# Optimization experiments

Hardware: AMD Instinct MI355X
Metric: run time of the kernel (lower is better)

Reference implementation:

```python
import jax, jax.numpy as jnp
import numpy as np
from jax import lax

DN = ('NCHW', 'OIHW', 'NCHW')

def conv3x3(x, w):
    return lax.conv_general_dilated(x, w, (1, 1), 'SAME', dimension_numbers=DN)

def conv1x1(x, w, b):
    # w: [O, C], x: [B, C, H, W]
    return jnp.einsum('oc,bchw->bohw', w, x) + b[None, :, None, None]

def bn_relu(x, p):
    # p: [2, C] -> (scale, shift), eval-mode folded BatchNorm + ReLU
    return jax.nn.relu(x * p[0][None, :, None, None] + p[1][None, :, None, None])

def pam(y, Wb, bb, Wc, bc, Wd, bd, alpha):
    B, C, H, W = y.shape
    n = H * W
    b_ = conv1x1(y, Wb, bb).reshape(B, -1, n)   # [B, C/8, N]
    c_ = conv1x1(y, Wc, bc).reshape(B, -1, n)   # [B, C/8, N]
    d_ = conv1x1(y, Wd, bd).reshape(B, C, n)    # [B, C, N]
    energy = jnp.einsum('bkn,bkm->bnm', b_, c_)  # [B, N, N]
    attn = jax.nn.softmax(energy, axis=-1)
    feat = jnp.einsum('bcm,bnm->bcn', d_, attn).reshape(B, C, H, W)
    return alpha[0] * feat + y

def cam(y, beta):
    B, C, H, W = y.shape
    xf = y.reshape(B, C, H * W)
    energy = jnp.einsum('bcn,bdn->bcd', xf, xf)  # [B, C, C]
    energy = jnp.max(energy, axis=-1, keepdims=True) - energy
    attn = jax.nn.softmax(energy, axis=-1)
    feat = jnp.einsum('bcd,bdn->bcn', attn, xf).reshape(B, C, H, W)
    return beta[0] * feat + y

def reference(x, Wp1, bnp1, Wc1, bnc1, Wb, bb, Wc, bc, Wd, bd, alpha, beta,
              Wp2, bnp2, Wc2, bnc2, Wout, bout, Wp3, bp3, Wc3, bc3):
    feat_p = bn_relu(conv3x3(x, Wp1), bnp1)
    feat_p = pam(feat_p, Wb, bb, Wc, bc, Wd, bd, alpha)
    feat_p = bn_relu(conv3x3(feat_p, Wp2), bnp2)

    feat_c = bn_relu(conv3x3(x, Wc1), bnc1)
    feat_c = cam(feat_c, beta)
    feat_c = bn_relu(conv3x3(feat_c, Wc2), bnc2)

    fusion = feat_p + feat_c
    out_main = jax.nn.sigmoid(conv1x1(fusion, Wout, bout))
    out_p = jax.nn.sigmoid(conv1x1(feat_p, Wp3, bp3))
    out_c = jax.nn.sigmoid(conv1x1(feat_c, Wc3, bc3))
    return (out_main, out_p, out_c)

def setup_inputs() -> dict:
    key = jax.random.key(0)
    ks = jax.random.split(key, 24)
    Cin, Ci, Ck, NC = 512, 128, 16, 19
    B, H, W = 8, 64, 64
    s = lambda k, shape, scale=0.05: jax.random.normal(k, shape, jnp.float32) * scale
    return {
        'x': jax.random.normal(ks[0], (B, Cin, H, W), jnp.float32),
        'Wp1': s(ks[1], (Ci, Cin, 3, 3)), 'bnp1': jnp.stack([jnp.ones(Ci), jnp.zeros(Ci)]),
        'Wc1': s(ks[2], (Ci, Cin, 3, 3)), 'bnc1': jnp.stack([jnp.ones(Ci), jnp.zeros(Ci)]),
        'Wb': s(ks[3], (Ck, Ci)), 'bb': s(ks[4], (Ck,)),
        'Wc': s(ks[5], (Ck, Ci)), 'bc': s(ks[6], (Ck,)),
        'Wd': s(ks[7], (Ci, Ci)), 'bd': s(ks[8], (Ci,)),
        'alpha': jax.random.normal(ks[9], (1,), jnp.float32) * 0.5,
        'beta': jax.random.normal(ks[10], (1,), jnp.float32) * 0.5,
        'Wp2': s(ks[11], (Ci, Ci, 3, 3)), 'bnp2': jnp.stack([jnp.ones(Ci), jnp.zeros(Ci)]),
        'Wc2': s(ks[12], (Ci, Ci, 3, 3)), 'bnc2': jnp.stack([jnp.ones(Ci), jnp.zeros(Ci)]),
        'Wout': s(ks[13], (NC, Ci)), 'bout': s(ks[14], (NC,)),
        'Wp3': s(ks[15], (NC, Ci)), 'bp3': s(ks[16], (NC,)),
        'Wc3': s(ks[17], (NC, Ci)), 'bc3': s(ks[18], (NC,)),
    }
```

## Files before the change

### kernel.cpp

```cpp
#include <hip/hip_runtime.h>
#include <math.h>


typedef __attribute__((ext_vector_type(8)))  short short8;
typedef __attribute__((ext_vector_type(16))) float f32x16;

__device__ inline unsigned short f2bf(float f) {
    union { float f; unsigned u; } v; v.f = f;
    unsigned r = v.u + 0x7fffu + ((v.u >> 16) & 1u);
    return (unsigned short)(r >> 16);
}
__device__ inline float bf2f(unsigned short h) {
    union { unsigned u; float f; } v; v.u = ((unsigned)h) << 16;
    return v.f;
}

__global__ __launch_bounds__(256) void wpack_kernel(
    const float* __restrict__ W, unsigned short* __restrict__ wp, int Cin, int total)
{
    int idx = blockIdx.x * 256 + threadIdx.x;
    if (idx >= total) return;
    int chunk = idx / 18432;
    int rem   = idx - chunk * 18432;
    int tap   = rem >> 11;
    int rem2  = rem & 2047;
    int g     = rem2 >> 10;
    int co    = (rem2 >> 3) & 127;
    int ci8   = rem2 & 7;
    int cin   = (chunk << 4) + (g << 3) + ci8;
    wp[idx] = f2bf(W[((size_t)co * Cin + cin) * 9 + tap]);
}

__global__ __launch_bounds__(256) void wpack_split_kernel(
    const float* __restrict__ W, unsigned short* __restrict__ wph,
    unsigned short* __restrict__ wpl, int Cin, int total)
{
    int idx = blockIdx.x * 256 + threadIdx.x;
    if (idx >= total) return;
    int chunk = idx / 18432;
    int rem   = idx - chunk * 18432;
    int tap   = rem >> 11;
    int rem2  = rem & 2047;
    int g     = rem2 >> 10;
    int co    = (rem2 >> 3) & 127;
    int ci8   = rem2 & 7;
    int cin   = (chunk << 4) + (g << 3) + ci8;
    float w = W[((size_t)co * Cin + cin) * 9 + tap];
    unsigned short hi = f2bf(w);
    wph[idx] = hi;
    wpl[idx] = f2bf(w - bf2f(hi));
}

__global__ __launch_bounds__(256, 4) void conv3x3_merged(
    const float* __restrict__ xin,
    const unsigned short* __restrict__ wpp,
    const unsigned short* __restrict__ wph, const unsigned short* __restrict__ wpl,
    const float* __restrict__ bnp, const float* __restrict__ bnc,
    float* __restrict__ outP, float* __restrict__ outC,
    unsigned short* __restrict__ outh, unsigned short* __restrict__ outl)
{
    const int t   = threadIdx.x;
    const int w2  = t >> 6;
    const int xh  = w2 & 1;
    const int wy  = w2 >> 1;
    const int ln  = t & 63;
    const int l31 = ln & 31;
    const int g   = ln >> 5;
    const int y   = blockIdx.x;
    const int co0 = blockIdx.y << 6;
    const int b   = blockIdx.z;

    const int sr   = t >> 6;
    const int sx   = t & 63;
    const int sgy  = y - 1 + sr;
    const bool sv  = (t < 192) && ((unsigned)sgy < 64u);
    const int spid = sr * 66 + sx + 1;

    __shared__ __align__(16) unsigned short Xh[2][3168];
    __shared__ __align__(16) unsigned short Xo[2][3168];

    for (int i = t; i < 792; i += 256) {
        uint4 z; z.x = 0; z.y = 0; z.z = 0; z.w = 0;
        ((uint4*)Xh)[i] = z;
        ((uint4*)Xo)[i] = z;
    }

    const int co = co0 + (wy << 5) + l31;
    const unsigned short* wPb = wpp + (size_t)(g << 10) + ((size_t)co << 3);
    const unsigned short* wHb = wph + (size_t)(g << 10) + ((size_t)co << 3);
    const unsigned short* wLb = wpl + (size_t)(g << 10) + ((size_t)co << 3);
    const float* xsrc = xin + ((size_t)b << 21) + (sgy << 6) + sx;

    const f32x16 zero = {0,0,0,0,0,0,0,0,0,0,0,0,0,0,0,0};
    f32x16 ap = zero, ac = zero;

    float xv[16];
    if (sv) {
#pragma unroll
        for (int c = 0; c < 16; c++) xv[c] = xsrc[(size_t)c << 12];
    }
    __syncthreads();

    if (sv) {
        unsigned short th[16], tl[16];
#pragma unroll
        for (int c = 0; c < 16; c++) {
            unsigned short hi = f2bf(xv[c]);
            th[c] = hi; tl[c] = f2bf(xv[c] - bf2f(hi));
        }
        *(uint4*)&Xh[0][spid << 3]          = ((uint4*)th)[0];
        *(uint4*)&Xh[0][1584 + (spid << 3)] = ((uint4*)th)[1];
        *(uint4*)&Xo[0][spid << 3]          = ((uint4*)tl)[0];
        *(uint4*)&Xo[0][1584 + (spid << 3)] = ((uint4*)tl)[1];
    }

    int cur = 0;
    for (int ch = 0; ch < 32; ++ch) {
        __syncthreads();
        const bool pf = (ch < 31);
        if (pf && sv) {
#pragma unroll
            for (int c = 0; c < 16; c++)
                xv[c] = xsrc[((size_t)(ch + 1) << 16) + ((size_t)c << 12)];
        }
        const size_t wo = (size_t)ch * 18432;
#pragma unroll 3
        for (int tap = 0; tap < 9; ++tap) {
            const int dy = tap / 3, dx = tap - dy * 3;
            const int xi = (g ? 1584 : 0) + (((dy * 66) + (xh << 5) + l31 + dx) << 3);
            short8 vap = *(const short8*)(wPb + wo + tap * 2048);
            short8 vah = *(const short8*)(wHb + wo + tap * 2048);
            short8 val = *(const short8*)(wLb + wo + tap * 2048);
            short8 bh_ = *(const short8*)&Xh[cur][xi];
            short8 bl_ = *(const short8*)&Xo[cur][xi];
            ap = __builtin_amdgcn_mfma_f32_32x32x16_bf16(vap, bh_, ap, 0, 0, 0);
            ac = __builtin_amdgcn_mfma_f32_32x32x16_bf16(vah, bh_, ac, 0, 0, 0);
            ac = __builtin_amdgcn_mfma_f32_32x32x16_bf16(vah, bl_, ac, 0, 0, 0);
            ac = __builtin_amdgcn_mfma_f32_32x32x16_bf16(val, bh_, ac, 0, 0, 0);
        }
        if (pf && sv) {
            unsigned short th[16], tl[16];
#pragma unroll
            for (int c = 0; c < 16; c++) {
                unsigned short hi = f2bf(xv[c]);
                th[c] = hi; tl[c] = f2bf(xv[c] - bf2f(hi));
            }
            const int nb = cur ^ 1;
            *(uint4*)&Xh[nb][spid << 3]          = ((uint4*)th)[0];
            *(uint4*)&Xh[nb][1584 + (spid << 3)] = ((uint4*)th)[1];
            *(uint4*)&Xo[nb][spid << 3]          = ((uint4*)tl)[0];
            *(uint4*)&Xo[nb][1584 + (spid << 3)] = ((uint4*)tl)[1];
        }
        cur ^= 1;
    }

    const int x = (xh << 5) + l31;
#pragma unroll
    for (int r = 0; r < 16; r++) {
        int c2 = co0 + (wy << 5) + (r & 3) + ((r >> 2) << 3) + (g << 2);
        size_t o = (((size_t)b * 128 + c2) << 12) + (y << 6) + x;
        float vp = fmaf(ap[r], bnp[c2], bnp[128 + c2]);
        vp = vp > 0.f ? vp : 0.f;
        outP[o] = vp;
        float vc = fmaf(ac[r], bnc[c2], bnc[128 + c2]);
        vc = vc > 0.f ? vc : 0.f;
        outC[o] = vc;
        unsigned short hi = f2bf(vc);
        outh[o] = hi;
        outl[o] = f2bf(vc - bf2f(hi));
    }
}

__global__ __launch_bounds__(256, 4) void conv3x3_bf(
    const unsigned short* __restrict__ xin, int Cin,
    const unsigned short* __restrict__ wpk, const float* __restrict__ bn,
    float* __restrict__ out_f32)
{
    const int t   = threadIdx.x;
    const int w2  = t >> 6;
    const int xh  = w2 & 1;
    const int wy  = w2 >> 1;
    const int ln  = t & 63;
    const int l31 = ln & 31;
    const int g   = ln >> 5;
    const int y   = blockIdx.x;
    const int co0 = blockIdx.y << 6;
    const int b   = blockIdx.z;

    const int sr   = t >> 6;
    const int sx   = t & 63;
    const int sgy  = y - 1 + sr;
    const bool sv  = (t < 192) && ((unsigned)sgy < 64u);
    const int spid = sr * 66 + sx + 1;

    __shared__ __align__(16) unsigned short Xl[2][3168];

    for (int i = t; i < 792; i += 256) {
        uint4 z; z.x = 0; z.y = 0; z.z = 0; z.w = 0;
        ((uint4*)Xl)[i] = z;
    }

    const int co = co0 + (wy << 5) + l31;
    const unsigned short* wB = wpk + (size_t)(g << 10) + ((size_t)co << 3);
    const unsigned short* xsrc = xin + (((size_t)b * Cin) << 12) + (sgy << 6) + sx;

    const f32x16 zero = {0,0,0,0,0,0,0,0,0,0,0,0,0,0,0,0};
    f32x16 acc = zero;

    unsigned short xv[16];
    if (sv) {
#pragma unroll
        for (int c = 0; c < 16; c++) xv[c] = xsrc[(size_t)c << 12];
    }
    __syncthreads();

    if (sv) {
        *(uint4*)&Xl[0][spid << 3]          = ((uint4*)xv)[0];
        *(uint4*)&Xl[0][1584 + (spid << 3)] = ((uint4*)xv)[1];
    }

    const int nchunks = Cin >> 4;
    int cur = 0;
    for (int ch = 0; ch < nchunks; ++ch) {
        __syncthreads();
        const bool pf = (ch < nchunks - 1);
        if (pf && sv) {
#pragma unroll
            for (int c = 0; c < 16; c++)
                xv[c] = xsrc[((size_t)(ch + 1) << 16) + ((size_t)c << 12)];
        }
        const size_t wo = (size_t)ch * 18432;
#pragma unroll 3
        for (int tap = 0; tap < 9; ++tap) {
            const int dy = tap / 3, dx = tap - dy * 3;
            const int xi = (g ? 1584 : 0) + (((dy * 66) + (xh << 5) + l31 + dx) << 3);
            short8 a  = *(const short8*)(wB + wo + tap * 2048);
            short8 b0 = *(const short8*)&Xl[cur][xi];
            acc = __builtin_amdgcn_mfma_f32_32x32x16_bf16(a, b0, acc, 0, 0, 0);
        }
        if (pf && sv) {
            const int nb = cur ^ 1;
            *(uint4*)&Xl[nb][spid << 3]          = ((uint4*)xv)[0];
            *(uint4*)&Xl[nb][1584 + (spid << 3)] = ((uint4*)xv)[1];
        }
        cur ^= 1;
    }

    const int x = (xh << 5) + l31;
#pragma unroll
    for (int r = 0; r < 16; r++) {
        int c2 = co0 + (wy << 5) + (r & 3) + ((r >> 2) << 3) + (g << 2);
        float v = fmaf(acc[r], bn[c2], bn[128 + c2]);
        v = v > 0.f ? v : 0.f;
        out_f32[(((size_t)b * 128 + c2) << 12) + (y << 6) + x] = v;
    }
}

__global__ __launch_bounds__(256, 4) void conv3x3_hilo_bf(
    const unsigned short* __restrict__ xhg, const unsigned short* __restrict__ xlg,
    int Cin, const unsigned short* __restrict__ wph, const unsigned short* __restrict__ wpl,
    const float* __restrict__ bn, float* __restrict__ out_f32)
{
    const int t   = threadIdx.x;
    const int w2  = t >> 6;
    const int xh  = w2 & 1;
    const int wy  = w2 >> 1;
    const int ln  = t & 63;
    const int l31 = ln & 31;
    const int g   = ln >> 5;
    const int y   = blockIdx.x;
    const int co0 = blockIdx.y << 6;
    const int b   = blockIdx.z;

    const int sr   = t >> 6;
    const int sx   = t & 63;
    const int sgy  = y - 1 + sr;
    const bool sv  = (t < 192) && ((unsigned)sgy < 64u);
    const int spid = sr * 66 + sx + 1;

    __shared__ __align__(16) unsigned short Xh[2][3168];
    __shared__ __align__(16) unsigned short Xo[2][3168];

    for (int i = t; i < 792; i += 256) {
        uint4 z; z.x = 0; z.y = 0; z.z = 0; z.w = 0;
        ((uint4*)Xh)[i] = z;
        ((uint4*)Xo)[i] = z;
    }

    const int co = co0 + (wy << 5) + l31;
    const unsigned short* wHb = wph + (size_t)(g << 10) + ((size_t)co << 3);
    const unsigned short* wLb = wpl + (size_t)(g << 10) + ((size_t)co << 3);
    const unsigned short* hsrc = xhg + (((size_t)b * Cin) << 12) + (sgy << 6) + sx;
    const unsigned short* lsrc = xlg + (((size_t)b * Cin) << 12) + (sgy << 6) + sx;

    const f32x16 zero = {0,0,0,0,0,0,0,0,0,0,0,0,0,0,0,0};
    f32x16 acc = zero;

    unsigned short hv[16], lv[16];
    if (sv) {
#pragma unroll
        for (int c = 0; c < 16; c++) { hv[c] = hsrc[(size_t)c << 12]; lv[c] = lsrc[(size_t)c << 12]; }
    }
    __syncthreads();

    if (sv) {
        *(uint4*)&Xh[0][spid << 3]          = ((uint4*)hv)[0];
        *(uint4*)&Xh[0][1584 + (spid << 3)] = ((uint4*)hv)[1];
        *(uint4*)&Xo[0][spid << 3]          = ((uint4*)lv)[0];
        *(uint4*)&Xo[0][1584 + (spid << 3)] = ((uint4*)lv)[1];
    }

    const int nchunks = Cin >> 4;
    int cur = 0;
    for (int ch = 0; ch < nchunks; ++ch) {
        __syncthreads();
        const bool pf = (ch < nchunks - 1);
        if (pf && sv) {
#pragma unroll
            for (int c = 0; c < 16; c++) {
                hv[c] = hsrc[((size_t)(ch + 1) << 16) + ((size_t)c << 12)];
                lv[c] = lsrc[((size_t)(ch + 1) << 16) + ((size_t)c << 12)];
            }
        }
        const size_t wo = (size_t)ch * 18432;
#pragma unroll 3
        for (int tap = 0; tap < 9; ++tap) {
            const int dy = tap / 3, dx = tap - dy * 3;
            const int xi = (g ? 1584 : 0) + (((dy * 66) + (xh << 5) + l31 + dx) << 3);
            short8 ah  = *(const short8*)(wHb + wo + tap * 2048);
            short8 al  = *(const short8*)(wLb + wo + tap * 2048);
            short8 bh_ = *(const short8*)&Xh[cur][xi];
            short8 bl_ = *(const short8*)&Xo[cur][xi];
            acc = __builtin_amdgcn_mfma_f32_32x32x16_bf16(ah, bh_, acc, 0, 0, 0);
            acc = __builtin_amdgcn_mfma_f32_32x32x16_bf16(ah, bl_, acc, 0, 0, 0);
            acc = __builtin_amdgcn_mfma_f32_32x32x16_bf16(al, bh_, acc, 0, 0, 0);
        }
        if (pf && sv) {
            const int nb = cur ^ 1;
            *(uint4*)&Xh[nb][spid << 3]          = ((uint4*)hv)[0];
            *(uint4*)&Xh[nb][1584 + (spid << 3)] = ((uint4*)hv)[1];
            *(uint4*)&Xo[nb][spid << 3]          = ((uint4*)lv)[0];
            *(uint4*)&Xo[nb][1584 + (spid << 3)] = ((uint4*)lv)[1];
        }
        cur ^= 1;
    }

    const int x = (xh << 5) + l31;
#pragma unroll
    for (int r = 0; r < 16; r++) {
        int c2 = co0 + (wy << 5) + (r & 3) + ((r >> 2) << 3) + (g << 2);
        float v = fmaf(acc[r], bn[c2], bn[128 + c2]);
        v = v > 0.f ? v : 0.f;
        out_f32[(((size_t)b * 128 + c2) << 12) + (y << 6) + x] = v;
    }
}

__global__ __launch_bounds__(256) void cam_energy_mfma(
    const unsigned short* __restrict__ bh, const unsigned short* __restrict__ bl,
    float* __restrict__ egy_part)
{
    const int t   = threadIdx.x;
    const int w   = t >> 6;
    const int ln  = t & 63;
    const int l31 = ln & 31;
    const int g   = ln >> 5;
    const int i0  = (blockIdx.x >> 2) << 5;
    const int j0  = (blockIdx.x & 3) << 5;
    const int nseg = blockIdx.y;
    const int b   = blockIdx.z;

    __shared__ float red[4][64][17];

    const f32x16 zero = {0,0,0,0,0,0,0,0,0,0,0,0,0,0,0,0};
    f32x16 acc = zero;
    const int nb = (nseg << 9) + (w << 7) + (g << 3);
    const size_t ri = ((size_t)b * 128 + i0 + l31) << 12;
    const size_t rj = ((size_t)b * 128 + j0 + l31) << 12;

#pragma unroll
    for (int c = 0; c < 8; c++) {
        const int n0 = nb + (c << 4);
        short8 ah  = *(const short8*)(bh + ri + n0);
        short8 al  = *(const short8*)(bl + ri + n0);
        short8 bhf = *(const short8*)(bh + rj + n0);
        short8 blf = *(const short8*)(bl + rj + n0);
        acc = __builtin_amdgcn_mfma_f32_32x32x16_bf16(ah, bhf, acc, 0, 0, 0);
        acc = __builtin_amdgcn_mfma_f32_32x32x16_bf16(ah, blf, acc, 0, 0, 0);
        acc = __builtin_amdgcn_mfma_f32_32x32x16_bf16(al, bhf, acc, 0, 0, 0);
    }
#pragma unroll
    for (int r = 0; r < 16; r++) red[w][ln][r] = acc[r];
    __syncthreads();

    const int lane = t & 63;
    const int rq   = t >> 6;
    float* base = egy_part + (((size_t)(nseg * 8 + b)) << 14);
#pragma unroll
    for (int e = 0; e < 4; e++) {
        const int reg = (rq << 2) + e;
        float v = red[0][lane][reg] + red[1][lane][reg]
                + red[2][lane][reg] + red[3][lane][reg];
        const int i = i0 + (reg & 3) + ((reg >> 2) << 3) + ((lane >> 5) << 2);
        base[i * 128 + j0 + (lane & 31)] = v;
    }
}

__global__ __launch_bounds__(256) void cam_softmax_fused(
    const float* __restrict__ egy_part, float* __restrict__ egy)
{
    const int b   = blockIdx.x;
    const int rg  = blockIdx.y;
    const int t   = threadIdx.x;
    const int row = (rg << 4) + (t >> 4);
    const int jg  = t & 15;

    float e[8];
#pragma unroll
    for (int jj = 0; jj < 8; jj++) e[jj] = 0.f;
    for (int seg = 0; seg < 8; seg++) {
        const float* p = egy_part + (((size_t)(seg * 8 + b)) << 14) + row * 128 + (jg << 3);
#pragma unroll
        for (int jj = 0; jj < 8; jj++) e[jj] += p[jj];
    }
    float mn = e[0];
#pragma unroll
    for (int jj = 1; jj < 8; jj++) mn = fminf(mn, e[jj]);
#pragma unroll
    for (int k = 1; k < 16; k <<= 1) mn = fminf(mn, __shfl_xor(mn, k));
    float s = 0.f;
#pragma unroll
    for (int jj = 0; jj < 8; jj++) { float p = __expf(mn - e[jj]); e[jj] = p; s += p; }
#pragma unroll
    for (int k = 1; k < 16; k <<= 1) s += __shfl_xor(s, k);
    const float inv = 1.f / s;
    float* orow = egy + ((size_t)b << 14) + row * 128 + (jg << 3);
#pragma unroll
    for (int jj = 0; jj < 8; jj++) orow[jj] = e[jj] * inv;
}

__global__ __launch_bounds__(256) void pam_qk_1x1(
    const float* __restrict__ A, const float* __restrict__ Wb, const float* __restrict__ bb,
    const float* __restrict__ Wc, const float* __restrict__ bc,
    unsigned short* __restrict__ qt, unsigned short* __restrict__ kt)
{
    __shared__ float wl[2 * 16 * 128];
    __shared__ float bl[32];
    const int t = threadIdx.x;
    const int n = (blockIdx.x << 8) + t;
    const int b = blockIdx.y;
    for (int idx = t; idx < 2048; idx += 256) { wl[idx] = Wb[idx]; wl[2048 + idx] = Wc[idx]; }
    if (t < 16) { bl[t] = bb[t]; bl[16 + t] = bc[t]; }
    __syncthreads();
    float ab[16], ac[16];
#pragma unroll
    for (int k = 0; k < 16; k++) { ab[k] = 0.f; ac[k] = 0.f; }
    for (int chn = 0; chn < 128; ++chn) {
        float a = A[(((size_t)b * 128 + chn) << 12) + n];
#pragma unroll
        for (int k = 0; k < 16; k++) {
            ab[k] = fmaf(wl[k * 128 + chn], a, ab[k]);
            ac[k] = fmaf(wl[2048 + k * 128 + chn], a, ac[k]);
        }
    }
    unsigned short uq[16], uk[16];
#pragma unroll
    for (int k = 0; k < 16; k++) {
        uq[k] = f2bf(ab[k] + bl[k]);
        uk[k] = f2bf(ac[k] + bl[16 + k]);
    }
    size_t row = (size_t)b * 4096 + n;
    ((uint4*)qt)[row * 2 + 0] = ((uint4*)uq)[0];
    ((uint4*)qt)[row * 2 + 1] = ((uint4*)uq)[1];
    ((uint4*)kt)[row * 2 + 0] = ((uint4*)uk)[0];
    ((uint4*)kt)[row * 2 + 1] = ((uint4*)uk)[1];
}

__global__ __launch_bounds__(256) void pam_v_1x1(
    const float* __restrict__ A, const float* __restrict__ Wd, const float* __restrict__ bd,
    unsigned short* __restrict__ vb)
{
    __shared__ float wl[32 * 128];
    __shared__ float bl[32];
    const int t   = threadIdx.x;
    const int n   = (blockIdx.x << 8) + t;
    const int co0 = blockIdx.y << 5;
    const int b   = blockIdx.z;
    for (int idx = t; idx < 4096; idx += 256) {
        int c2 = idx >> 7, chv = idx & 127;
        wl[idx] = Wd[(co0 + c2) * 128 + chv];
    }
    if (t < 32) bl[t] = bd[co0 + t];
    __syncthreads();
    float acc[32];
#pragma unroll
    for (int k = 0; k < 32; k++) acc[k] = 0.f;
    for (int chn = 0; chn < 128; ++chn) {
        float a = A[(((size_t)b * 128 + chn) << 12) + n];
#pragma unroll
        for (int k = 0; k < 32; k++) acc[k] = fmaf(wl[k * 128 + chn], a, acc[k]);
    }
#pragma unroll
    for (int k = 0; k < 32; k++)
        vb[(((size_t)b * 128 + co0 + k) << 12) + n] = f2bf(acc[k] + bl[k]);
}

__global__ __launch_bounds__(256) void pam_attn_mfma(
    const unsigned short* __restrict__ qt, const unsigned short* __restrict__ kt,
    const unsigned short* __restrict__ vb,
    const float* __restrict__ alpha, const float* __restrict__ Y,
    unsigned short* __restrict__ outb)
{
    const int t  = threadIdx.x;
    const int w  = t >> 6;
    const int L  = t & 63;
    const int ln = L & 31;
    const int g  = L >> 5;
    const int b  = blockIdx.y;
    const int n0 = blockIdx.x << 5;
    const int c0 = w << 5;

    __shared__ unsigned short Pf[16 * 256];
    __shared__ float red[4][32];

    const f32x16 zero = {0,0,0,0,0,0,0,0,0,0,0,0,0,0,0,0};
    short8 qfrag = *(const short8*)(qt + (((size_t)b * 4096 + n0 + ln) << 4) + (g << 3));
    const float al = alpha[0];

    f32x16 acc = zero;
    float rs = 0.f;
    float mold = -3.0e38f;

    for (int m0 = 0; m0 < 4096; m0 += 128) {
        const int mq = m0 + (w << 5);
        short8 kfrag = *(const short8*)(kt + (((size_t)b * 4096 + mq + ln) << 4) + (g << 3));
        f32x16 s = __builtin_amdgcn_mfma_f32_32x32x16_bf16(kfrag, qfrag, zero, 0, 0, 0);

        float lm = s[0];
#pragma unroll
        for (int r = 1; r < 16; r++) lm = fmaxf(lm, s[r]);
        lm = fmaxf(lm, __shfl_xor(lm, 32));
        if (L < 32) red[w][L] = lm;
        __syncthreads();
        const float mb = fmaxf(fmaxf(red[0][ln], red[1][ln]),
                               fmaxf(red[2][ln], red[3][ln]));
        const float mnew = fmaxf(mold, mb);
        const float fs = __expf(mold - mnew);
        mold = mnew;
        rs *= fs;
#pragma unroll
        for (int r = 0; r < 16; r++) acc[r] *= fs;

        float p[16];
#pragma unroll
        for (int r = 0; r < 16; r++) { p[r] = __expf(s[r] - mnew); rs += p[r]; }
        float xx[16];
#pragma unroll
        for (int r = 0; r < 16; r++) xx[r] = __shfl_xor(p[r], 32);

        unsigned short f0[8], f1[8];
#pragma unroll
        for (int i = 0; i < 4; i++) {
            f0[i]     = f2bf(g ? xx[4 + i]  : p[i]);
            f0[4 + i] = f2bf(g ? p[4 + i]   : xx[i]);
            f1[i]     = f2bf(g ? xx[12 + i] : p[8 + i]);
            f1[4 + i] = f2bf(g ? p[12 + i]  : xx[8 + i]);
        }
        *(short8*)(&Pf[((w << 2) + g) * 256 + (ln << 3)])     = *(short8*)f0;
        *(short8*)(&Pf[((w << 2) + 2 + g) * 256 + (ln << 3)]) = *(short8*)f1;
        __syncthreads();

#pragma unroll
        for (int kk = 0; kk < 8; kk++) {
            short8 pfrag = *(const short8*)(&Pf[((kk << 1) + g) * 256 + (ln << 3)]);
            short8 vfrag = *(const short8*)(vb + (((size_t)b * 128 + c0 + ln) << 12)
                                               + m0 + (kk << 4) + (g << 3));
            acc = __builtin_amdgcn_mfma_f32_32x32x16_bf16(vfrag, pfrag, acc, 0, 0, 0);
        }
        __syncthreads();
    }

    rs += __shfl_xor(rs, 32);
    if (L < 32) red[w][L] = rs;
    __syncthreads();
    const float inv = 1.f / (red[0][ln] + red[1][ln] + red[2][ln] + red[3][ln]);
    const int n = n0 + ln;
#pragma unroll
    for (int r = 0; r < 16; r++) {
        int c = c0 + (r & 3) + ((r >> 2) << 3) + (g << 2);
        size_t idx = (((size_t)b * 128 + c) << 12) + n;
        outb[idx] = f2bf(fmaf(al, acc[r] * inv, Y[idx]));
    }
}

__global__ __launch_bounds__(256) void cam_feat(
    const float* __restrict__ attn, const float* __restrict__ Bf,
    const float* __restrict__ beta, unsigned short* __restrict__ oh,
    unsigned short* __restrict__ ol)
{
    const int t  = threadIdx.x;
    const int n  = (blockIdx.x << 8) + t;
    const int c0 = blockIdx.y << 5;
    const int b  = blockIdx.z;
    __shared__ float al[32 * 128];
    for (int idx = t; idx < 4096; idx += 256)
        al[idx] = attn[(size_t)b * 16384 + (c0 + (idx >> 7)) * 128 + (idx & 127)];
    __syncthreads();
    float acc[32];
#pragma unroll
    for (int k = 0; k < 32; k++) acc[k] = 0.f;
    for (int d = 0; d < 128; ++d) {
        float v = Bf[(((size_t)b * 128 + d) << 12) + n];
#pragma unroll
        for (int k = 0; k < 32; k++) acc[k] = fmaf(al[k * 128 + d], v, acc[k]);
    }
    float be = beta[0];
#pragma unroll
    for (int k = 0; k < 32; k++) {
        size_t idx = (((size_t)b * 128 + c0 + k) << 12) + n;
        float v = fmaf(be, acc[k], Bf[idx]);
        unsigned short hi = f2bf(v);
        oh[idx] = hi;
        ol[idx] = f2bf(v - bf2f(hi));
    }
}

__global__ __launch_bounds__(256) void heads(
    const float* __restrict__ FP, const float* __restrict__ FC,
    const float* __restrict__ Wout, const float* __restrict__ bout,
    const float* __restrict__ Wp3, const float* __restrict__ bp3,
    const float* __restrict__ Wc3, const float* __restrict__ bc3,
    float* __restrict__ out)
{
    const int t = threadIdx.x;
    const int n = (blockIdx.x << 8) + t;
    const int b = blockIdx.y;
    __shared__ float wl[3 * 19 * 128];
    __shared__ float bl[3 * 19];
    for (int idx = t; idx < 2432; idx += 256) {
        wl[idx]        = Wout[idx];
        wl[2432 + idx] = Wp3[idx];
        wl[4864 + idx] = Wc3[idx];
    }
    if (t < 19) { bl[t] = bout[t]; bl[19 + t] = bp3[t]; bl[38 + t] = bc3[t]; }
    __syncthreads();
    float am[19], ap[19], ac[19];
#pragma unroll
    for (int o = 0; o < 19; o++) { am[o] = 0.f; ap[o] = 0.f; ac[o] = 0.f; }
    for (int chn = 0; chn < 128; ++chn) {
        float pv = FP[(((size_t)b * 128 + chn) << 12) + n];
        float cv = FC[(((size_t)b * 128 + chn) << 12) + n];
        float fv = pv + cv;
#pragma unroll
        for (int o = 0; o < 19; o++) {
            am[o] = fmaf(wl[o * 128 + chn], fv, am[o]);
            ap[o] = fmaf(wl[2432 + o * 128 + chn], pv, ap[o]);
            ac[o] = fmaf(wl[4864 + o * 128 + chn], cv, ac[o]);
        }
    }
    const size_t OS = (size_t)8 * 19 * 4096;
#pragma unroll
    for (int o = 0; o < 19; o++) {
        size_t base = (((size_t)b * 19 + o) << 12) + n;
        out[base]          = 1.f / (1.f + __expf(-(am[o] + bl[o])));
        out[OS + base]     = 1.f / (1.f + __expf(-(ap[o] + bl[19 + o])));
        out[2 * OS + base] = 1.f / (1.f + __expf(-(ac[o] + bl[38 + o])));
    }
}

extern "C" void kernel_launch(void* const* d_in, const int* in_sizes, int n_in,
                              void* d_out, int out_size, void* d_ws, size_t ws_size,
                              hipStream_t stream)
{
    const float* x     = (const float*)d_in[0];
    const float* Wp1   = (const float*)d_in[1];
    const float* bnp1  = (const float*)d_in[2];
    const float* Wc1   = (const float*)d_in[3];
    const float* bnc1  = (const float*)d_in[4];
    const float* Wb    = (const float*)d_in[5];
    const float* bb    = (const float*)d_in[6];
    const float* Wc    = (const float*)d_in[7];
    const float* bcv   = (const float*)d_in[8];
    const float* Wd    = (const float*)d_in[9];
    const float* bd    = (const float*)d_in[10];
    const float* alpha = (const float*)d_in[11];
    const float* beta  = (const float*)d_in[12];
    const float* Wp2   = (const float*)d_in[13];
    const float* bnp2  = (const float*)d_in[14];
    const float* Wc2   = (const float*)d_in[15];
    const float* bnc2  = (const float*)d_in[16];
    const float* Wout  = (const float*)d_in[17];
    const float* bo    = (const float*)d_in[18];
    const float* Wp3   = (const float*)d_in[19];
    const float* bp3   = (const float*)d_in[20];
    const float* Wc3   = (const float*)d_in[21];
    const float* bc3   = (const float*)d_in[22];
    float* out = (float*)d_out;

    char* ws = (char*)d_ws;
    const size_t MB = 1u << 20;
    const size_t W1SZ = (size_t)32 * 18432 * 2;
    const size_t W2SZ = (size_t)8 * 18432 * 2;
    float*          bufA     = (float*)(ws);
    float*          bufB     = (float*)(ws + 16 * MB);
    unsigned short* vb       = (unsigned short*)(ws + 32 * MB);
    float*          egy_part = (float*)(ws + 40 * MB);
    float*          bufD     = (float*)(ws + 32 * MB);
    unsigned short* bh       = (unsigned short*)(ws + 48 * MB);
    unsigned short* blo      = (unsigned short*)(ws + 56 * MB);
    unsigned short* pam_bf   = (unsigned short*)(ws + 48 * MB);
    unsigned short* c2h      = (unsigned short*)(ws + 48 * MB);
    unsigned short* c2l      = (unsigned short*)(ws + 56 * MB);
    unsigned short* qt       = (unsigned short*)(ws + 64 * MB);
    unsigned short* kt       = (unsigned short*)(ws + 65 * MB);
    float*          egy      = (float*)(ws + 66 * MB + (1u << 17));
    unsigned short* wp1      = (unsigned short*)(ws + 67 * MB);
    unsigned short* wc1h     = (unsigned short*)(ws + 67 * MB + W1SZ);
    unsigned short* wc1l     = (unsigned short*)(ws + 67 * MB + 2 * W1SZ);
    unsigned short* wp2      = (unsigned short*)(ws + 67 * MB + 3 * W1SZ);
    unsigned short* wc2h     = (unsigned short*)(ws + 67 * MB + 3 * W1SZ + W2SZ);
    unsigned short* wc2l     = (unsigned short*)(ws + 67 * MB + 3 * W1SZ + 2 * W2SZ);

    dim3 blk(256);
    const int n1 = 32 * 18432;
    const int n2 = 8 * 18432;
    wpack_kernel<<<dim3((n1 + 255) / 256), blk, 0, stream>>>(Wp1, wp1, 512, n1);
    wpack_kernel<<<dim3((n2 + 255) / 256), blk, 0, stream>>>(Wp2, wp2, 128, n2);
    wpack_split_kernel<<<dim3((n1 + 255) / 256), blk, 0, stream>>>(Wc1, wc1h, wc1l, 512, n1);
    wpack_split_kernel<<<dim3((n2 + 255) / 256), blk, 0, stream>>>(Wc2, wc2h, wc2l, 128, n2);

    conv3x3_merged<<<dim3(64, 2, 8), blk, 0, stream>>>(x, wp1, wc1h, wc1l, bnp1, bnc1,
                                                       bufA, bufB, bh, blo);
    cam_energy_mfma<<<dim3(16, 8, 8), blk, 0, stream>>>(bh, blo, egy_part);
    cam_softmax_fused<<<dim3(8, 8), blk, 0, stream>>>(egy_part, egy);
    pam_qk_1x1<<<dim3(16, 8), blk, 0, stream>>>(bufA, Wb, bb, Wc, bcv, qt, kt);
    pam_v_1x1<<<dim3(16, 4, 8), blk, 0, stream>>>(bufA, Wd, bd, vb);
    pam_attn_mfma<<<dim3(128, 8), blk, 0, stream>>>(qt, kt, vb, alpha, bufA, pam_bf);
    conv3x3_bf<<<dim3(64, 2, 8), blk, 0, stream>>>(pam_bf, 128, wp2, bnp2, bufD);
    cam_feat<<<dim3(16, 4, 8), blk, 0, stream>>>(egy, bufB, beta, c2h, c2l);
    conv3x3_hilo_bf<<<dim3(64, 2, 8), blk, 0, stream>>>(c2h, c2l, 128, wc2h, wc2l, bnc2, bufA);
    heads<<<dim3(16, 8), blk, 0, stream>>>(bufD, bufA, Wout, bo, Wp3, bp3, Wc3, bc3, out);
}
```

Before: 757.6 us.

## Split-K the first conv pair and merge both second convs into one launch

```diff
diff --git a/kernel.cpp b/kernel.cpp
--- a/kernel.cpp
+++ b/kernel.cpp
@@ -51,13 +51,11 @@
     wpl[idx] = f2bf(w - bf2f(hi));
 }
 
-__global__ __launch_bounds__(256, 4) void conv3x3_merged(
+__global__ __launch_bounds__(256, 4) void conv1_ksplit(
     const float* __restrict__ xin,
     const unsigned short* __restrict__ wpp,
     const unsigned short* __restrict__ wph, const unsigned short* __restrict__ wpl,
-    const float* __restrict__ bnp, const float* __restrict__ bnc,
-    float* __restrict__ outP, float* __restrict__ outC,
-    unsigned short* __restrict__ outh, unsigned short* __restrict__ outl)
+    float* __restrict__ partP, float* __restrict__ partC)
 {
     const int t   = threadIdx.x;
     const int w2  = t >> 6;
@@ -67,7 +65,8 @@
     const int l31 = ln & 31;
     const int g   = ln >> 5;
     const int y   = blockIdx.x;
-    const int co0 = blockIdx.y << 6;
+    const int co0 = (blockIdx.y & 1) << 6;
+    const int kh  = blockIdx.y >> 1;
     const int b   = blockIdx.z;
 
     const int sr   = t >> 6;
@@ -89,7 +88,8 @@
     const unsigned short* wPb = wpp + (size_t)(g << 10) + ((size_t)co << 3);
     const unsigned short* wHb = wph + (size_t)(g << 10) + ((size_t)co << 3);
     const unsigned short* wLb = wpl + (size_t)(g << 10) + ((size_t)co << 3);
-    const float* xsrc = xin + ((size_t)b << 21) + (sgy << 6) + sx;
+    const float* xsrc = xin + ((size_t)b << 21) + (((size_t)(kh << 8)) << 12)
+                            + (sgy << 6) + sx;
 
     const f32x16 zero = {0,0,0,0,0,0,0,0,0,0,0,0,0,0,0,0};
     f32x16 ap = zero, ac = zero;
@@ -115,15 +115,15 @@
     }
 
     int cur = 0;
-    for (int ch = 0; ch < 32; ++ch) {
+    for (int ch = 0; ch < 16; ++ch) {
         __syncthreads();
-        const bool pf = (ch < 31);
+        const bool pf = (ch < 15);
         if (pf && sv) {
 #pragma unroll
             for (int c = 0; c < 16; c++)
                 xv[c] = xsrc[((size_t)(ch + 1) << 16) + ((size_t)c << 12)];
         }
-        const size_t wo = (size_t)ch * 18432;
+        const size_t wo = (size_t)((kh << 4) + ch) * 18432;
 #pragma unroll 3
         for (int tap = 0; tap < 9; ++tap) {
             const int dy = tap / 3, dx = tap - dy * 3;
@@ -155,26 +155,67 @@
     }
 
     const int x = (xh << 5) + l31;
+    float* pP = partP + (size_t)kh * 4194304;
+    float* pC = partC + (size_t)kh * 4194304;
 #pragma unroll
     for (int r = 0; r < 16; r++) {
         int c2 = co0 + (wy << 5) + (r & 3) + ((r >> 2) << 3) + (g << 2);
         size_t o = (((size_t)b * 128 + c2) << 12) + (y << 6) + x;
-        float vp = fmaf(ap[r], bnp[c2], bnp[128 + c2]);
-        vp = vp > 0.f ? vp : 0.f;
-        outP[o] = vp;
-        float vc = fmaf(ac[r], bnc[c2], bnc[128 + c2]);
-        vc = vc > 0.f ? vc : 0.f;
-        outC[o] = vc;
-        unsigned short hi = f2bf(vc);
-        outh[o] = hi;
-        outl[o] = f2bf(vc - bf2f(hi));
-    }
-}
-
-__global__ __launch_bounds__(256, 4) void conv3x3_bf(
-    const unsigned short* __restrict__ xin, int Cin,
-    const unsigned short* __restrict__ wpk, const float* __restrict__ bn,
-    float* __restrict__ out_f32)
+        pP[o] = ap[r];
+        pC[o] = ac[r];
+    }
+}
+
+__global__ __launch_bounds__(256) void conv1_finalize(
+    const float* P, const float* C,
+    const float* bnp, const float* bnc,
+    float* A, float* Bf, unsigned short* bh2, unsigned short* bl2)
+{
+    const size_t i0 = ((((size_t)blockIdx.x << 8) + threadIdx.x) << 3);
+    const int c = (int)((i0 >> 12) & 127);
+    const float sp = bnp[c], tp = bnp[128 + c];
+    const float sc = bnc[c], tc = bnc[128 + c];
+
+    float p0[8], p1[8], c0[8], c1[8];
+    *(float4*)&p0[0] = *(const float4*)(P + i0);
+    *(float4*)&p0[4] = *(const float4*)(P + i0 + 4);
+    *(float4*)&p1[0] = *(const float4*)(P + 4194304 + i0);
+    *(float4*)&p1[4] = *(const float4*)(P + 4194304 + i0 + 4);
+    *(float4*)&c0[0] = *(const float4*)(C + i0);
+    *(float4*)&c0[4] = *(const float4*)(C + i0 + 4);
+    *(float4*)&c1[0] = *(const float4*)(C + 4194304 + i0);
+    *(float4*)&c1[4] = *(const float4*)(C + 4194304 + i0 + 4);
+
+    float vp[8], vc[8];
+    unsigned short hh[8], ll[8];
+#pragma unroll
+    for (int k = 0; k < 8; k++) {
+        float sP = p0[k] + p1[k];
+        float v = fmaf(sP, sp, tp);
+        vp[k] = v > 0.f ? v : 0.f;
+        float sC = c0[k] + c1[k];
+        float w = fmaf(sC, sc, tc);
+        w = w > 0.f ? w : 0.f;
+        vc[k] = w;
+        unsigned short hi = f2bf(w);
+        hh[k] = hi;
+        ll[k] = f2bf(w - bf2f(hi));
+    }
+    *(float4*)(A + i0)      = *(float4*)&vp[0];
+    *(float4*)(A + i0 + 4)  = *(float4*)&vp[4];
+    *(float4*)(Bf + i0)     = *(float4*)&vc[0];
+    *(float4*)(Bf + i0 + 4) = *(float4*)&vc[4];
+    *(uint4*)(bh2 + (i0 << 1)) = *(uint4*)hh;
+    *(uint4*)(bl2 + (i0 << 1)) = *(uint4*)ll;
+}
+
+__global__ __launch_bounds__(256, 4) void conv2_combo(
+    const unsigned short* __restrict__ xp,
+    const unsigned short* __restrict__ xch, const unsigned short* __restrict__ xcl,
+    const unsigned short* __restrict__ wpp, const unsigned short* __restrict__ wph,
+    const unsigned short* __restrict__ wpl,
+    const float* __restrict__ bnp, const float* __restrict__ bnc,
+    float* __restrict__ outP, float* __restrict__ outC)
 {
     const int t   = threadIdx.x;
     const int w2  = t >> 6;
@@ -184,7 +225,8 @@
     const int l31 = ln & 31;
     const int g   = ln >> 5;
     const int y   = blockIdx.x;
-    const int co0 = blockIdx.y << 6;
+    const int mode = blockIdx.y >> 1;
+    const int co0  = (blockIdx.y & 1) << 6;
     const int b   = blockIdx.z;
 
     const int sr   = t >> 6;
@@ -193,165 +235,127 @@
     const bool sv  = (t < 192) && ((unsigned)sgy < 64u);
     const int spid = sr * 66 + sx + 1;
 
-    __shared__ __align__(16) unsigned short Xl[2][3168];
+    __shared__ __align__(16) unsigned short Xa[2][3168];
+    __shared__ __align__(16) unsigned short Xb[2][3168];
 
     for (int i = t; i < 792; i += 256) {
         uint4 z; z.x = 0; z.y = 0; z.z = 0; z.w = 0;
-        ((uint4*)Xl)[i] = z;
+        ((uint4*)Xa)[i] = z;
+        ((uint4*)Xb)[i] = z;
     }
 
     const int co = co0 + (wy << 5) + l31;
-    const unsigned short* wB = wpk + (size_t)(g << 10) + ((size_t)co << 3);
-    const unsigned short* xsrc = xin + (((size_t)b * Cin) << 12) + (sgy << 6) + sx;
-
     const f32x16 zero = {0,0,0,0,0,0,0,0,0,0,0,0,0,0,0,0};
     f32x16 acc = zero;
-
-    unsigned short xv[16];
-    if (sv) {
-#pragma unroll
-        for (int c = 0; c < 16; c++) xv[c] = xsrc[(size_t)c << 12];
-    }
-    __syncthreads();
-
-    if (sv) {
-        *(uint4*)&Xl[0][spid << 3]          = ((uint4*)xv)[0];
-        *(uint4*)&Xl[0][1584 + (spid << 3)] = ((uint4*)xv)[1];
-    }
-
-    const int nchunks = Cin >> 4;
-    int cur = 0;
-    for (int ch = 0; ch < nchunks; ++ch) {
+    const int x = (xh << 5) + l31;
+
+    if (mode == 0) {
+        const unsigned short* wB = wpp + (size_t)(g << 10) + ((size_t)co << 3);
+        const unsigned short* xsrc = xp + ((size_t)b << 19) + (sgy << 6) + sx;
+
+        unsigned short xv[16];
+        if (sv) {
+#pragma unroll
+            for (int c = 0; c < 16; c++) xv[c] = xsrc[(size_t)c << 12];
+        }
         __syncthreads();
-        const bool pf = (ch < nchunks - 1);
-        if (pf && sv) {
-#pragma unroll
-            for (int c = 0; c < 16; c++)
-                xv[c] = xsrc[((size_t)(ch + 1) << 16) + ((size_t)c << 12)];
-        }
-        const size_t wo = (size_t)ch * 18432;
+        if (sv) {
+            *(uint4*)&Xa[0][spid << 3]          = ((uint4*)xv)[0];
+            *(uint4*)&Xa[0][1584 + (spid << 3)] = ((uint4*)xv)[1];
+        }
+        int cur = 0;
+        for (int ch = 0; ch < 8; ++ch) {
+            __syncthreads();
+            const bool pf = (ch < 7);
+            if (pf && sv) {
+#pragma unroll
+                for (int c = 0; c < 16; c++)
+                    xv[c] = xsrc[((size_t)(ch + 1) << 16) + ((size_t)c << 12)];
+            }
+            const size_t wo = (size_t)ch * 18432;
 #pragma unroll 3
-        for (int tap = 0; tap < 9; ++tap) {
-            const int dy = tap / 3, dx = tap - dy * 3;
-            const int xi = (g ? 1584 : 0) + (((dy * 66) + (xh << 5) + l31 + dx) << 3);
-            short8 a  = *(const short8*)(wB + wo + tap * 2048);
-            short8 b0 = *(const short8*)&Xl[cur][xi];
-            acc = __builtin_amdgcn_mfma_f32_32x32x16_bf16(a, b0, acc, 0, 0, 0);
-        }
-        if (pf && sv) {
-            const int nb = cur ^ 1;
-            *(uint4*)&Xl[nb][spid << 3]          = ((uint4*)xv)[0];
-            *(uint4*)&Xl[nb][1584 + (spid << 3)] = ((uint4*)xv)[1];
-        }
-        cur ^= 1;
-    }
-
-    const int x = (xh << 5) + l31;
-#pragma unroll
-    for (int r = 0; r < 16; r++) {
-        int c2 = co0 + (wy << 5) + (r & 3) + ((r >> 2) << 3) + (g << 2);
-        float v = fmaf(acc[r], bn[c2], bn[128 + c2]);
-        v = v > 0.f ? v : 0.f;
-        out_f32[(((size_t)b * 128 + c2) << 12) + (y << 6) + x] = v;
-    }
-}
-
-__global__ __launch_bounds__(256, 4) void conv3x3_hilo_bf(
-    const unsigned short* __restrict__ xhg, const unsigned short* __restrict__ xlg,
-    int Cin, const unsigned short* __restrict__ wph, const unsigned short* __restrict__ wpl,
-    const float* __restrict__ bn, float* __restrict__ out_f32)
-{
-    const int t   = threadIdx.x;
-    const int w2  = t >> 6;
-    const int xh  = w2 & 1;
-    const int wy  = w2 >> 1;
-    const int ln  = t & 63;
-    const int l31 = ln & 31;
-    const int g   = ln >> 5;
-    const int y   = blockIdx.x;
-    const int co0 = blockIdx.y << 6;
-    const int b   = blockIdx.z;
-
-    const int sr   = t >> 6;
-    const int sx   = t & 63;
-    const int sgy  = y - 1 + sr;
-    const bool sv  = (t < 192) && ((unsigned)sgy < 64u);
-    const int spid = sr * 66 + sx + 1;
-
-    __shared__ __align__(16) unsigned short Xh[2][3168];
-    __shared__ __align__(16) unsigned short Xo[2][3168];
-
-    for (int i = t; i < 792; i += 256) {
-        uint4 z; z.x = 0; z.y = 0; z.z = 0; z.w = 0;
-        ((uint4*)Xh)[i] = z;
-        ((uint4*)Xo)[i] = z;
-    }
-
-    const int co = co0 + (wy << 5) + l31;
-    const unsigned short* wHb = wph + (size_t)(g << 10) + ((size_t)co << 3);
-    const unsigned short* wLb = wpl + (size_t)(g << 10) + ((size_t)co << 3);
-    const unsigned short* hsrc = xhg + (((size_t)b * Cin) << 12) + (sgy << 6) + sx;
-    const unsigned short* lsrc = xlg + (((size_t)b * Cin) << 12) + (sgy << 6) + sx;
-
-    const f32x16 zero = {0,0,0,0,0,0,0,0,0,0,0,0,0,0,0,0};
-    f32x16 acc = zero;
-
-    unsigned short hv[16], lv[16];
-    if (sv) {
-#pragma unroll
-        for (int c = 0; c < 16; c++) { hv[c] = hsrc[(size_t)c << 12]; lv[c] = lsrc[(size_t)c << 12]; }
-    }
-    __syncthreads();
-
-    if (sv) {
-        *(uint4*)&Xh[0][spid << 3]          = ((uint4*)hv)[0];
-        *(uint4*)&Xh[0][1584 + (spid << 3)] = ((uint4*)hv)[1];
-        *(uint4*)&Xo[0][spid << 3]          = ((uint4*)lv)[0];
-        *(uint4*)&Xo[0][1584 + (spid << 3)] = ((uint4*)lv)[1];
-    }
-
-    const int nchunks = Cin >> 4;
-    int cur = 0;
-    for (int ch = 0; ch < nchunks; ++ch) {
+            for (int tap = 0; tap < 9; ++tap) {
+                const int dy = tap / 3, dx = tap - dy * 3;
+                const int xi = (g ? 1584 : 0) + (((dy * 66) + (xh << 5) + l31 + dx) << 3);
+                short8 a  = *(const short8*)(wB + wo + tap * 2048);
+                short8 b0 = *(const short8*)&Xa[cur][xi];
+                acc = __builtin_amdgcn_mfma_f32_32x32x16_bf16(a, b0, acc, 0, 0, 0);
+            }
+            if (pf && sv) {
+                const int nb = cur ^ 1;
+                *(uint4*)&Xa[nb][spid << 3]          = ((uint4*)xv)[0];
+                *(uint4*)&Xa[nb][1584 + (spid << 3)] = ((uint4*)xv)[1];
+            }
+            cur ^= 1;
+        }
+#pragma unroll
+        for (int r = 0; r < 16; r++) {
+            int c2 = co0 + (wy << 5) + (r & 3) + ((r >> 2) << 3) + (g << 2);
+            float v = fmaf(acc[r], bnp[c2], bnp[128 + c2]);
+            v = v > 0.f ? v : 0.f;
+            outP[(((size_t)b * 128 + c2) << 12) + (y << 6) + x] = v;
+        }
+    } else {
+        const unsigned short* wHb = wph + (size_t)(g << 10) + ((size_t)co << 3);
+        const unsigned short* wLb = wpl + (size_t)(g << 10) + ((size_t)co << 3);
+        const unsigned short* hsrc = xch + ((size_t)b << 19) + (sgy << 6) + sx;
+        const unsigned short* lsrc = xcl + ((size_t)b << 19) + (sgy << 6) + sx;
+
+        unsigned short hv[16], lv[16];
+        if (sv) {
+#pragma unroll
+            for (int c = 0; c < 16; c++) {
+                hv[c] = hsrc[(size_t)c << 12];
+                lv[c] = lsrc[(size_t)c << 12];
+            }
+        }
         __syncthreads();
-        const bool pf = (ch < nchunks - 1);
-        if (pf && sv) {
-#pragma unroll
-            for (int c = 0; c < 16; c++) {
-                hv[c] = hsrc[((size_t)(ch + 1) << 16) + ((size_t)c << 12)];
-                lv[c] = lsrc[((size_t)(ch + 1) << 16) + ((size_t)c << 12)];
+        if (sv) {
+            *(uint4*)&Xa[0][spid << 3]          = ((uint4*)hv)[0];
+            *(uint4*)&Xa[0][1584 + (spid << 3)] = ((uint4*)hv)[1];
+            *(uint4*)&Xb[0][spid << 3]          = ((uint4*)lv)[0];
+            *(uint4*)&Xb[0][1584 + (spid << 3)] = ((uint4*)lv)[1];
+        }
+        int cur = 0;
+        for (int ch = 0; ch < 8; ++ch) {
+            __syncthreads();
+            const bool pf = (ch < 7);
+            if (pf && sv) {
+#pragma unroll
+                for (int c = 0; c < 16; c++) {
+                    hv[c] = hsrc[((size_t)(ch + 1) << 16) + ((size_t)c << 12)];
+                    lv[c] = lsrc[((size_t)(ch + 1) << 16) + ((size_t)c << 12)];
+                }
             }
-        }
-        const size_t wo = (size_t)ch * 18432;
+            const size_t wo = (size_t)ch * 18432;
 #pragma unroll 3
-        for (int tap = 0; tap < 9; ++tap) {
-            const int dy = tap / 3, dx = tap - dy * 3;
-            const int xi = (g ? 1584 : 0) + (((dy * 66) + (xh << 5) + l31 + dx) << 3);
-            short8 ah  = *(const short8*)(wHb + wo + tap * 2048);
-            short8 al  = *(const short8*)(wLb + wo + tap * 2048);
-            short8 bh_ = *(const short8*)&Xh[cur][xi];
-            short8 bl_ = *(const short8*)&Xo[cur][xi];
-            acc = __builtin_amdgcn_mfma_f32_32x32x16_bf16(ah, bh_, acc, 0, 0, 0);
-            acc = __builtin_amdgcn_mfma_f32_32x32x16_bf16(ah, bl_, acc, 0, 0, 0);
-            acc = __builtin_amdgcn_mfma_f32_32x32x16_bf16(al, bh_, acc, 0, 0, 0);
-        }
-        if (pf && sv) {
-            const int nb = cur ^ 1;
-            *(uint4*)&Xh[nb][spid << 3]          = ((uint4*)hv)[0];
-            *(uint4*)&Xh[nb][1584 + (spid << 3)] = ((uint4*)hv)[1];
-            *(uint4*)&Xo[nb][spid << 3]          = ((uint4*)lv)[0];
-            *(uint4*)&Xo[nb][1584 + (spid << 3)] = ((uint4*)lv)[1];
-        }
-        cur ^= 1;
-    }
-
-    const int x = (xh << 5) + l31;
-#pragma unroll
-    for (int r = 0; r < 16; r++) {
-        int c2 = co0 + (wy << 5) + (r & 3) + ((r >> 2) << 3) + (g << 2);
-        float v = fmaf(acc[r], bn[c2], bn[128 + c2]);
-        v = v > 0.f ? v : 0.f;
-        out_f32[(((size_t)b * 128 + c2) << 12) + (y << 6) + x] = v;
+            for (int tap = 0; tap < 9; ++tap) {
+                const int dy = tap / 3, dx = tap - dy * 3;
+                const int xi = (g ? 1584 : 0) + (((dy * 66) + (xh << 5) + l31 + dx) << 3);
+                short8 ah  = *(const short8*)(wHb + wo + tap * 2048);
+                short8 al  = *(const short8*)(wLb + wo + tap * 2048);
+                short8 bh_ = *(const short8*)&Xa[cur][xi];
+                short8 bl_ = *(const short8*)&Xb[cur][xi];
+                acc = __builtin_amdgcn_mfma_f32_32x32x16_bf16(ah, bh_, acc, 0, 0, 0);
+                acc = __builtin_amdgcn_mfma_f32_32x32x16_bf16(ah, bl_, acc, 0, 0, 0);
+                acc = __builtin_amdgcn_mfma_f32_32x32x16_bf16(al, bh_, acc, 0, 0, 0);
+            }
+            if (pf && sv) {
+                const int nb = cur ^ 1;
+                *(uint4*)&Xa[nb][spid << 3]          = ((uint4*)hv)[0];
+                *(uint4*)&Xa[nb][1584 + (spid << 3)] = ((uint4*)hv)[1];
+                *(uint4*)&Xb[nb][spid << 3]          = ((uint4*)lv)[0];
+                *(uint4*)&Xb[nb][1584 + (spid << 3)] = ((uint4*)lv)[1];
+            }
+            cur ^= 1;
+        }
+#pragma unroll
+        for (int r = 0; r < 16; r++) {
+            int c2 = co0 + (wy << 5) + (r & 3) + ((r >> 2) << 3) + (g << 2);
+            float v = fmaf(acc[r], bnc[c2], bnc[128 + c2]);
+            v = v > 0.f ? v : 0.f;
+            outC[(((size_t)b * 128 + c2) << 12) + (y << 6) + x] = v;
+        }
     }
 }
 
@@ -374,16 +378,16 @@
     const f32x16 zero = {0,0,0,0,0,0,0,0,0,0,0,0,0,0,0,0};
     f32x16 acc = zero;
     const int nb = (nseg << 9) + (w << 7) + (g << 3);
-    const size_t ri = ((size_t)b * 128 + i0 + l31) << 12;
-    const size_t rj = ((size_t)b * 128 + j0 + l31) << 12;
+    const size_t ri = ((size_t)b * 128 + i0 + l31) << 13;
+    const size_t rj = ((size_t)b * 128 + j0 + l31) << 13;
 
 #pragma unroll
     for (int c = 0; c < 8; c++) {
-        const int n0 = nb + (c << 4);
-        short8 ah  = *(const short8*)(bh + ri + n0);
-        short8 al  = *(const short8*)(bl + ri + n0);
-        short8 bhf = *(const short8*)(bh + rj + n0);
-        short8 blf = *(const short8*)(bl + rj + n0);
+        const int n2 = (nb + (c << 4)) << 1;
+        short8 ah  = *(const short8*)(bh + ri + n2);
+        short8 al  = *(const short8*)(bl + ri + n2);
+        short8 bhf = *(const short8*)(bh + rj + n2);
+        short8 blf = *(const short8*)(bl + rj + n2);
         acc = __builtin_amdgcn_mfma_f32_32x32x16_bf16(ah, bhf, acc, 0, 0, 0);
         acc = __builtin_amdgcn_mfma_f32_32x32x16_bf16(ah, blf, acc, 0, 0, 0);
         acc = __builtin_amdgcn_mfma_f32_32x32x16_bf16(al, bhf, acc, 0, 0, 0);
@@ -698,27 +702,30 @@
 
     char* ws = (char*)d_ws;
     const size_t MB = 1u << 20;
-    const size_t W1SZ = (size_t)32 * 18432 * 2;
-    const size_t W2SZ = (size_t)8 * 18432 * 2;
-    float*          bufA     = (float*)(ws);
-    float*          bufB     = (float*)(ws + 16 * MB);
-    unsigned short* vb       = (unsigned short*)(ws + 32 * MB);
-    float*          egy_part = (float*)(ws + 40 * MB);
-    float*          bufD     = (float*)(ws + 32 * MB);
-    unsigned short* bh       = (unsigned short*)(ws + 48 * MB);
-    unsigned short* blo      = (unsigned short*)(ws + 56 * MB);
-    unsigned short* pam_bf   = (unsigned short*)(ws + 48 * MB);
-    unsigned short* c2h      = (unsigned short*)(ws + 48 * MB);
-    unsigned short* c2l      = (unsigned short*)(ws + 56 * MB);
-    unsigned short* qt       = (unsigned short*)(ws + 64 * MB);
-    unsigned short* kt       = (unsigned short*)(ws + 65 * MB);
-    float*          egy      = (float*)(ws + 66 * MB + (1u << 17));
-    unsigned short* wp1      = (unsigned short*)(ws + 67 * MB);
-    unsigned short* wc1h     = (unsigned short*)(ws + 67 * MB + W1SZ);
-    unsigned short* wc1l     = (unsigned short*)(ws + 67 * MB + 2 * W1SZ);
-    unsigned short* wp2      = (unsigned short*)(ws + 67 * MB + 3 * W1SZ);
-    unsigned short* wc2h     = (unsigned short*)(ws + 67 * MB + 3 * W1SZ + W2SZ);
-    unsigned short* wc2l     = (unsigned short*)(ws + 67 * MB + 3 * W1SZ + 2 * W2SZ);
+    const size_t W1 = (size_t)32 * 18432;
+    const size_t W2 = (size_t)8 * 18432;
+
+    float*          partP  = (float*)(ws);
+    float*          partC  = (float*)(ws + 32 * MB);
+    float*          bufA   = (float*)(ws);
+    float*          bufB   = (float*)(ws + 16 * MB);
+    unsigned short* bh2    = (unsigned short*)(ws + 32 * MB);
+    unsigned short* bl2    = (unsigned short*)(ws + 48 * MB);
+    unsigned short* vb     = (unsigned short*)(ws + 32 * MB);
+    unsigned short* pam_bf = (unsigned short*)(ws + 40 * MB);
+    unsigned short* c2h    = (unsigned short*)(ws + 48 * MB);
+    unsigned short* c2l    = (unsigned short*)(ws + 56 * MB);
+    float*          bufD   = (float*)(ws + 16 * MB);
+    unsigned short* wp1    = (unsigned short*)(ws + 64 * MB);
+    unsigned short* wc1h   = wp1 + W1;
+    unsigned short* wc1l   = wc1h + W1;
+    float*          egy_part = (float*)(ws + 64 * MB);
+    unsigned short* wp2    = (unsigned short*)(ws + 68 * MB);
+    unsigned short* wc2h   = wp2 + W2;
+    unsigned short* wc2l   = wc2h + W2;
+    float*          egy    = (float*)(ws + 69 * MB);
+    unsigned short* qt     = (unsigned short*)(ws + 69 * MB + (1u << 19));
+    unsigned short* kt     = qt + (1u << 19);
 
     dim3 blk(256);
     const int n1 = 32 * 18432;
@@ -728,15 +735,17 @@
     wpack_split_kernel<<<dim3((n1 + 255) / 256), blk, 0, stream>>>(Wc1, wc1h, wc1l, 512, n1);
     wpack_split_kernel<<<dim3((n2 + 255) / 256), blk, 0, stream>>>(Wc2, wc2h, wc2l, 128, n2);
 
-    conv3x3_merged<<<dim3(64, 2, 8), blk, 0, stream>>>(x, wp1, wc1h, wc1l, bnp1, bnc1,
-                                                       bufA, bufB, bh, blo);
-    cam_energy_mfma<<<dim3(16, 8, 8), blk, 0, stream>>>(bh, blo, egy_part);
+    conv1_ksplit<<<dim3(64, 4, 8), blk, 0, stream>>>(x, wp1, wc1h, wc1l, partP, partC);
+    conv1_finalize<<<dim3(2048), blk, 0, stream>>>(partP, partC, bnp1, bnc1,
+                                                   bufA, bufB, bh2, bl2);
+    cam_energy_mfma<<<dim3(16, 8, 8), blk, 0, stream>>>(bh2, bl2, egy_part);
     cam_softmax_fused<<<dim3(8, 8), blk, 0, stream>>>(egy_part, egy);
+    cam_feat<<<dim3(16, 4, 8), blk, 0, stream>>>(egy, bufB, beta, c2h, c2l);
     pam_qk_1x1<<<dim3(16, 8), blk, 0, stream>>>(bufA, Wb, bb, Wc, bcv, qt, kt);
     pam_v_1x1<<<dim3(16, 4, 8), blk, 0, stream>>>(bufA, Wd, bd, vb);
     pam_attn_mfma<<<dim3(128, 8), blk, 0, stream>>>(qt, kt, vb, alpha, bufA, pam_bf);
-    conv3x3_bf<<<dim3(64, 2, 8), blk, 0, stream>>>(pam_bf, 128, wp2, bnp2, bufD);
-    cam_feat<<<dim3(16, 4, 8), blk, 0, stream>>>(egy, bufB, beta, c2h, c2l);
-    conv3x3_hilo_bf<<<dim3(64, 2, 8), blk, 0, stream>>>(c2h, c2l, 128, wc2h, wc2l, bnc2, bufA);
+    conv2_combo<<<dim3(64, 4, 8), blk, 0, stream>>>(pam_bf, c2h, c2l,
+                                                    wp2, wc2h, wc2l, bnp2, bnc2,
+                                                    bufD, bufA);
     heads<<<dim3(16, 8), blk, 0, stream>>>(bufD, bufA, Wout, bo, Wp3, bp3, Wc3, bc3, out);
 }
```

Result: slower. 788.7 us (+4.1%).
